# Performance work log

Measured on AMD Instinct MI355X. Metric: run time of the kernel, lower is better.

The kernel has to match this reference:

```python
import jax, jax.numpy as jnp
import numpy as np

# norse default LIFParameters
DT = 1e-3
TAU_SYN_INV = 200.0
TAU_MEM_INV = 100.0
V_LEAK = 0.0
V_TH = 1.0
V_RESET = 0.0


def heaviside(x):
    return (x > 0).astype(x.dtype)


def setup_inputs() -> dict:
    key = jax.random.key(0)
    ks = jax.random.split(key, 5)
    T, B, I, H, O = 14, 4096, 2048, 1024, 128
    x = (jax.random.uniform(ks[0], (T, B, I), dtype=jnp.float32) < 0.2).astype(jnp.float32)  # spike train
    w_in = jax.random.normal(ks[1], (H, I), dtype=jnp.float32) * (1.0 / np.sqrt(I))
    w_rec = jax.random.normal(ks[2], (H, H), dtype=jnp.float32) * (1.0 / np.sqrt(H))
    out_w = jax.random.normal(ks[3], (O, H), dtype=jnp.float32) * (1.0 / np.sqrt(H))
    out_b = jax.random.normal(ks[4], (O,), dtype=jnp.float32) * 0.01
    return {"x": x, "w_in": w_in, "w_rec": w_rec, "out_w": out_w, "out_b": out_b}


def reference(x, w_in, w_rec, out_w, out_b):
    T, B, _ = x.shape
    H = w_in.shape[0]
    z0 = jnp.zeros((B, H), dtype=x.dtype)
    v0 = jnp.full((B, H), V_LEAK, dtype=x.dtype)
    i0 = jnp.zeros((B, H), dtype=x.dtype)

    def step(carry, x_t):
        z, v, i = carry
        v_dec = v + DT * TAU_MEM_INV * ((V_LEAK - v) + i)   # membrane integration
        i_dec = i - DT * TAU_SYN_INV * i                    # synaptic decay
        z_new = heaviside(v_dec - V_TH)                     # spike
        v_new = (1.0 - z_new) * v_dec + z_new * V_RESET     # reset
        i_new = i_dec + x_t @ w_in.T + z @ w_rec.T          # input + recurrent current
        return (z_new, v_new, i_new), None

    (z_T, _, _), _ = jax.lax.scan(step, (z0, v0, i0), x)
    return z_T @ out_w.T + out_b
```

## Files before the change

kernel.cpp:

```cpp
#include <hip/hip_runtime.h>
#include <stdint.h>

#define T_STEPS 14
#define B_DIM   4096
#define I_DIM   2048
#define H_DIM   1024
#define O_DIM   128
#define K_TOT   3072

#define WSCALE_F 33554432.0f

typedef __bf16  bf16x8  __attribute__((ext_vector_type(8)));
typedef float   floatx4 __attribute__((ext_vector_type(4)));
typedef int     int4v   __attribute__((ext_vector_type(4)));
typedef int     int16v  __attribute__((ext_vector_type(16)));

__device__ __forceinline__ uint16_t f2bf_rne(float f) {
    uint32_t u = __float_as_uint(f);
    u += 0x7fffu + ((u >> 16) & 1u);
    return (uint16_t)(u >> 16);
}
__device__ __forceinline__ float bf2f(uint16_t h) {
    return __uint_as_float(((uint32_t)h) << 16);
}

__device__ __forceinline__ void gload_lds16(const void* g, void* l) {
    __builtin_amdgcn_global_load_lds((__attribute__((address_space(1))) void*)g,
                                     (__attribute__((address_space(3))) void*)l, 16, 0, 0);
}


__global__ void split_w_kernel(const float* __restrict__ w_in, const float* __restrict__ w_rec,
                               int8_t* __restrict__ WB) {
    int idx = blockIdx.x * 256 + threadIdx.x;
    int h = idx / K_TOT;
    int k = idx - h * K_TOT;
    float w = (k < I_DIM) ? w_in[(size_t)h * I_DIM + k]
                          : w_rec[(size_t)h * H_DIM + (k - I_DIM)];
    int W  = __float2int_rn(w * WSCALE_F);
    int d0 = (int8_t)(W & 0xFF);
    int r1 = (W - d0) >> 8;
    int d1 = (int8_t)(r1 & 0xFF);
    int d2 = (r1 - d1) >> 8;
    int nt = h >> 5, n32 = h & 31;
    int ktw = k >> 7, k128 = k & 127;
    int kk = k128 >> 5, half = (k128 >> 4) & 1, j = k128 & 15;
    int lane = half * 32 + n32;
    size_t base = (size_t)(nt * 24 + ktw) * 12288 + kk * 1024 + lane * 16 + j;
    WB[base] = (int8_t)d0; WB[base + 4096] = (int8_t)d1; WB[base + 8192] = (int8_t)d2;
}

__global__ void split_ow_kernel(const float* __restrict__ out_w, uint16_t* __restrict__ OW3) {
    int idx = blockIdx.x * 256 + threadIdx.x;
    float w = out_w[idx];
    uint16_t hi = f2bf_rne(w);
    float r1 = w - bf2f(hi);
    uint16_t mid = f2bf_rne(r1);
    float r2 = r1 - bf2f(mid);
    uint16_t lo = f2bf_rne(r2);
    const size_t S = (size_t)O_DIM * H_DIM;
    OW3[idx] = hi; OW3[idx + S] = mid; OW3[idx + 2 * S] = lo;
}

__global__ void cvt_x_kernel(const float* __restrict__ x, int8_t* __restrict__ xb) {
    size_t gid = (size_t)blockIdx.x * 256 + threadIdx.x;
    int g = (int)(gid & 1023);
    size_t chunk = gid >> 10;
    int kt   = (int)(chunk & 15);
    int mIdx = (int)((chunk >> 4) & 31);
    int t    = (int)(chunk >> 9);
    int group = g >> 8, kk = (g >> 6) & 3, lane = g & 63;
    int half = lane >> 5, row32 = lane & 31;
    int b = mIdx * 128 + group * 32 + row32;
    int k = kt * 128 + kk * 32 + half * 16;
    const float4* src = (const float4*)(x + ((size_t)t * B_DIM + b) * I_DIM + k);
    union { int8_t bytes[16]; int4v v; } u;
#pragma unroll
    for (int q = 0; q < 4; ++q) {
        float4 f = src[q];
        u.bytes[q * 4 + 0] = (int8_t)(f.x > 0.5f);
        u.bytes[q * 4 + 1] = (int8_t)(f.y > 0.5f);
        u.bytes[q * 4 + 2] = (int8_t)(f.z > 0.5f);
        u.bytes[q * 4 + 3] = (int8_t)(f.w > 0.5f);
    }
    ((int4v*)xb)[gid] = u.v;
}

__launch_bounds__(256, 4)
__global__ void lif_step_kernel(const int8_t* __restrict__ Xt,
                                const int8_t* __restrict__ Zin,
                                const int8_t* __restrict__ WB,
                                float2* __restrict__ VI,
                                int8_t* __restrict__ Zout,
                                uint16_t* __restrict__ Zbf, int t) {
    __shared__ int8_t sA[16384];
    __shared__ int8_t sB[12288];

    const int tid  = threadIdx.x;
    const int wave = tid >> 6, lane = tid & 63;
    const int lane32 = lane & 31, hl = lane >> 5;

    const int nt = blockIdx.x & 31, mIdx = blockIdx.x >> 5;
    const int mBase = mIdx * 128, nBase = nt * 32;

    int16v acc[3] = {};

    const int nIters = (t > 0) ? 24 : 16;

    for (int kt = 0; kt < nIters; ++kt) {
        __syncthreads();
        const int8_t* chunkA = (kt < 16)
            ? Xt  + ((size_t)mIdx * 16 + kt) * 16384
            : Zin + ((size_t)mIdx * 8 + (kt - 16)) * 16384;
#pragma unroll
        for (int j = 0; j < 4; ++j) {
            const int seg = j * 4 + wave;
            gload_lds16(chunkA + seg * 1024 + lane * 16, &sA[seg * 1024]);
        }
        const int8_t* chunkB = WB + (size_t)(nt * 24 + kt) * 12288;
#pragma unroll
        for (int j = 0; j < 3; ++j) {
            const int seg = j * 4 + wave;
            gload_lds16(chunkB + seg * 1024 + lane * 16, &sB[seg * 1024]);
        }
        __syncthreads();
#pragma unroll
        for (int kk = 0; kk < 4; ++kk) {
            int4v aF = *(const int4v*)&sA[wave * 4096 + kk * 1024 + lane * 16];
#pragma unroll
            for (int s = 0; s < 3; ++s) {
                int4v bF = *(const int4v*)&sB[s * 4096 + kk * 1024 + lane * 16];
                acc[s] = __builtin_amdgcn_mfma_i32_32x32x32_i8(aF, bF, acc[s], 0, 0, 0);
            }
        }
    }

    int8_t* zchunk = Zout + ((size_t)mIdx * 8 + (nt >> 2)) * 16384;
#pragma unroll
    for (int r = 0; r < 16; ++r) {
#pragma clang fp contract(off)
        float cur = (float)acc[2][r] * (1.0f / 512.0f)
                  + (float)acc[1][r] * (1.0f / 131072.0f)
                  + (float)acc[0][r] * (1.0f / 33554432.0f);
        int row = (r & 3) + 8 * (r >> 2) + 4 * hl;
        int b = mBase + wave * 32 + row;
        int h = nBase + lane32;
        size_t idx = (size_t)b * H_DIM + h;
        float v, ii;
        if (t == 0) { v = 0.0f; ii = 0.0f; }
        else        { float2 vi = VI[idx]; v = vi.x; ii = vi.y; }
        float v_dec = v + 0.1f * ((0.0f - v) + ii);
        float i_dec = ii - 0.2f * ii;
        bool z = (v_dec > 1.0f);
        float2 vi_new;
        vi_new.x = z ? 0.0f : v_dec;
        vi_new.y = i_dec + cur;
        VI[idx] = vi_new;
        if (t == T_STEPS - 1) {
            Zbf[idx] = z ? (uint16_t)0x3F80 : (uint16_t)0;
        } else {
            zchunk[wave * 4096 + (nt & 3) * 1024
                   + ((lane32 >> 4) * 32 + row) * 16 + (lane32 & 15)]
                = z ? (int8_t)1 : (int8_t)0;
        }
    }
}

__launch_bounds__(256)
__global__ void out_gemm_kernel(const uint16_t* __restrict__ Zfin,
                                const uint16_t* __restrict__ OW3,
                                const float* __restrict__ out_b,
                                float* __restrict__ out) {
    __shared__ uint16_t sA[16 * 32];
    __shared__ uint16_t sB[3][128 * 32];

    const int tid  = threadIdx.x;
    const int wave = tid >> 6, lane = tid & 63;
    const int quad = lane >> 4, col = lane & 15;

    const int mBase = blockIdx.x * 16;

    floatx4 acc[2] = {};

    const int ldRow = lane >> 2;
    const int ldCol = (lane & 3) * 8;

    for (int kt = 0; kt < H_DIM / 32; ++kt) {
        const int kb = kt * 32;
        __syncthreads();
        if (wave == 0) {
            const uint16_t* g = Zfin + (size_t)(mBase + ldRow) * H_DIM + kb + ldCol;
            gload_lds16(g, &sA[0]);
        }
#pragma unroll
        for (int s = 0; s < 3; ++s) {
            const uint16_t* wsrc = OW3 + (size_t)s * O_DIM * H_DIM;
#pragma unroll
            for (int j = 0; j < 2; ++j) {
                const int rseg = j * 4 + wave;
                const uint16_t* g = wsrc + (size_t)(rseg * 16 + ldRow) * H_DIM + kb + ldCol;
                gload_lds16(g, &sB[s][rseg * 16 * 32]);
            }
        }
        __syncthreads();

        bf16x8 aF = *reinterpret_cast<const bf16x8*>(&sA[col * 32 + quad * 8]);
#pragma unroll
        for (int s = 0; s < 3; ++s) {
#pragma unroll
            for (int ni = 0; ni < 2; ++ni) {
                int row = wave * 32 + ni * 16 + col;
                bf16x8 bF = *reinterpret_cast<const bf16x8*>(&sB[s][row * 32 + quad * 8]);
                acc[ni] = __builtin_amdgcn_mfma_f32_16x16x32_bf16(aF, bF, acc[ni], 0, 0, 0);
            }
        }
    }

    {
#pragma clang fp contract(off)
#pragma unroll
        for (int ni = 0; ni < 2; ++ni)
#pragma unroll
            for (int r = 0; r < 4; ++r) {
                int b = mBase + quad * 4 + r;
                int h = wave * 32 + ni * 16 + col;
                out[(size_t)b * O_DIM + h] = acc[ni][r] + out_b[h];
            }
    }
}

extern "C" void kernel_launch(void* const* d_in, const int* in_sizes, int n_in,
                              void* d_out, int out_size, void* d_ws, size_t ws_size,
                              hipStream_t stream) {
    const float* x     = (const float*)d_in[0];
    const float* w_in  = (const float*)d_in[1];
    const float* w_rec = (const float*)d_in[2];
    const float* out_w = (const float*)d_in[3];
    const float* out_b = (const float*)d_in[4];
    float* out = (float*)d_out;

    char* ws = (char*)d_ws;
    size_t off = 0;
    int8_t*   WB   = (int8_t*)(ws + off);   off += (size_t)3 * H_DIM * K_TOT;
    uint16_t* OW3  = (uint16_t*)(ws + off); off += (size_t)3 * O_DIM * H_DIM * 2;
    int8_t*   Xall = (int8_t*)(ws + off);   off += (size_t)T_STEPS * B_DIM * I_DIM;
    uint16_t* Zbf  = (uint16_t*)(ws + off); off += (size_t)B_DIM * H_DIM * 2;
    int8_t*   Z0   = (int8_t*)(ws + off);   off += (size_t)B_DIM * H_DIM;
    int8_t*   Z1   = (int8_t*)(ws + off);   off += (size_t)B_DIM * H_DIM;
    float2*   VI   = (float2*)(ws + off);   off += (size_t)B_DIM * H_DIM * 8;

    split_w_kernel<<<(H_DIM * K_TOT) / 256, 256, 0, stream>>>(w_in, w_rec, WB);
    split_ow_kernel<<<(O_DIM * H_DIM) / 256, 256, 0, stream>>>(out_w, OW3);
    cvt_x_kernel<<<(int)(((size_t)T_STEPS * B_DIM * I_DIM / 16) / 256), 256, 0, stream>>>(x, Xall);

    int8_t* zbuf[2] = { Z0, Z1 };
    for (int t = 0; t < T_STEPS; ++t) {
        lif_step_kernel<<<dim3(1024), 256, 0, stream>>>(
            Xall + (size_t)t * 32 * 16 * 16384, zbuf[t & 1], WB, VI,
            zbuf[(t + 1) & 1], Zbf, t);
    }
    out_gemm_kernel<<<B_DIM / 16, 256, 0, stream>>>(Zbf, OW3, out_b, out);
}
```

Before: 1.375 ms.

## Fuse LIF timesteps into one persistent cooperative kernel with grid sync

```diff
diff --git a/kernel.cpp b/kernel.cpp
--- a/kernel.cpp
+++ b/kernel.cpp
@@ -1,5 +1,8 @@
 #include <hip/hip_runtime.h>
+#include <hip/hip_cooperative_groups.h>
 #include <stdint.h>
+
+namespace cg = cooperative_groups;
 
 #define T_STEPS 14
 #define B_DIM   4096
@@ -84,6 +87,116 @@
         u.bytes[q * 4 + 3] = (int8_t)(f.w > 0.5f);
     }
     ((int4v*)xb)[gid] = u.v;
+}
+
+__launch_bounds__(256, 4)
+__global__ void lif_persist_kernel(const int8_t* __restrict__ Xall,
+                                   const int8_t* __restrict__ WB,
+                                   int8_t* __restrict__ Z0,
+                                   int8_t* __restrict__ Z1,
+                                   uint16_t* __restrict__ Zbf) {
+    __shared__ int8_t sA[16384];
+    __shared__ int8_t sB[12288];
+
+    const int tid  = threadIdx.x;
+    const int wave = tid >> 6, lane = tid & 63;
+    const int lane32 = lane & 31, hl = lane >> 5;
+
+    const int nt = blockIdx.x & 31, mIdx = blockIdx.x >> 5;
+    const int mBase = mIdx * 128, nBase = nt * 32;
+
+    float vmem[16], isyn[16];
+#pragma unroll
+    for (int r = 0; r < 16; ++r) { vmem[r] = 0.0f; isyn[r] = 0.0f; }
+
+    int8_t* zA = Z0;
+    int8_t* zB = Z1;
+
+    for (int t = 0; t < T_STEPS; ++t) {
+        int16v acc[3] = {};
+        const int8_t* Xt = Xall + (size_t)t * ((size_t)B_DIM * I_DIM);
+
+        for (int kt = 0; kt < 16; ++kt) {
+            __syncthreads();
+            const int8_t* chunkA = Xt + ((size_t)mIdx * 16 + kt) * 16384;
+#pragma unroll
+            for (int j = 0; j < 4; ++j) {
+                const int seg = j * 4 + wave;
+                gload_lds16(chunkA + seg * 1024 + lane * 16, &sA[seg * 1024]);
+            }
+            const int8_t* chunkB = WB + (size_t)(nt * 24 + kt) * 12288;
+#pragma unroll
+            for (int j = 0; j < 3; ++j) {
+                const int seg = j * 4 + wave;
+                gload_lds16(chunkB + seg * 1024 + lane * 16, &sB[seg * 1024]);
+            }
+            __syncthreads();
+#pragma unroll
+            for (int kk = 0; kk < 4; ++kk) {
+                int4v aF = *(const int4v*)&sA[wave * 4096 + kk * 1024 + lane * 16];
+#pragma unroll
+                for (int s = 0; s < 3; ++s) {
+                    int4v bF = *(const int4v*)&sB[s * 4096 + kk * 1024 + lane * 16];
+                    acc[s] = __builtin_amdgcn_mfma_i32_32x32x32_i8(aF, bF, acc[s], 0, 0, 0);
+                }
+            }
+        }
+
+        if (t > 0) {
+            cg::this_grid().sync();
+            for (int kt = 0; kt < 8; ++kt) {
+                __syncthreads();
+                const int8_t* chunkA = zA + ((size_t)mIdx * 8 + kt) * 16384;
+#pragma unroll
+                for (int j = 0; j < 4; ++j) {
+                    const int seg = j * 4 + wave;
+                    gload_lds16(chunkA + seg * 1024 + lane * 16, &sA[seg * 1024]);
+                }
+                const int8_t* chunkB = WB + (size_t)(nt * 24 + 16 + kt) * 12288;
+#pragma unroll
+                for (int j = 0; j < 3; ++j) {
+                    const int seg = j * 4 + wave;
+                    gload_lds16(chunkB + seg * 1024 + lane * 16, &sB[seg * 1024]);
+                }
+                __syncthreads();
+#pragma unroll
+                for (int kk = 0; kk < 4; ++kk) {
+                    int4v aF = *(const int4v*)&sA[wave * 4096 + kk * 1024 + lane * 16];
+#pragma unroll
+                    for (int s = 0; s < 3; ++s) {
+                        int4v bF = *(const int4v*)&sB[s * 4096 + kk * 1024 + lane * 16];
+                        acc[s] = __builtin_amdgcn_mfma_i32_32x32x32_i8(aF, bF, acc[s], 0, 0, 0);
+                    }
+                }
+            }
+        }
+
+        int8_t* zchunk = zB + ((size_t)mIdx * 8 + (nt >> 2)) * 16384;
+#pragma unroll
+        for (int r = 0; r < 16; ++r) {
+#pragma clang fp contract(off)
+            float cur = (float)acc[2][r] * (1.0f / 512.0f)
+                      + (float)acc[1][r] * (1.0f / 131072.0f)
+                      + (float)acc[0][r] * (1.0f / 33554432.0f);
+            int row = (r & 3) + 8 * (r >> 2) + 4 * hl;
+            float v_dec = vmem[r] + 0.1f * ((0.0f - vmem[r]) + isyn[r]);
+            float i_dec = isyn[r] - 0.2f * isyn[r];
+            bool z = (v_dec > 1.0f);
+            vmem[r] = z ? 0.0f : v_dec;
+            isyn[r] = i_dec + cur;
+            if (t == T_STEPS - 1) {
+                int b = mBase + wave * 32 + row;
+                int h = nBase + lane32;
+                Zbf[(size_t)b * H_DIM + h] = z ? (uint16_t)0x3F80 : (uint16_t)0;
+            } else {
+                zchunk[wave * 4096 + (nt & 3) * 1024
+                       + ((lane32 >> 4) * 32 + row) * 16 + (lane32 & 15)]
+                    = z ? (int8_t)1 : (int8_t)0;
+            }
+        }
+
+        int8_t* tmp = zA; zA = zB; zB = tmp;
+    }
 }
 
 __launch_bounds__(256, 4)
@@ -253,11 +366,30 @@
     split_ow_kernel<<<(O_DIM * H_DIM) / 256, 256, 0, stream>>>(out_w, OW3);
     cvt_x_kernel<<<(int)(((size_t)T_STEPS * B_DIM * I_DIM / 16) / 256), 256, 0, stream>>>(x, Xall);
 
-    int8_t* zbuf[2] = { Z0, Z1 };
-    for (int t = 0; t < T_STEPS; ++t) {
-        lif_step_kernel<<<dim3(1024), 256, 0, stream>>>(
-            Xall + (size_t)t * 32 * 16 * 16384, zbuf[t & 1], WB, VI,
-            zbuf[(t + 1) & 1], Zbf, t);
-    }
+    static int coop_ok = -1;
+    if (coop_ok < 0) {
+        int dev = 0, v = 0;
+        (void)hipGetDevice(&dev);
+        if (hipDeviceGetAttribute(&v, hipDeviceAttributeCooperativeLaunch, dev) != hipSuccess) v = 0;
+        coop_ok = v;
+    }
+
+    bool launched = false;
+    if (coop_ok) {
+        void* args[] = { (void*)&Xall, (void*)&WB, (void*)&Z0, (void*)&Z1, (void*)&Zbf };
+        hipError_t e = hipLaunchCooperativeKernel((const void*)lif_persist_kernel,
+                                                  dim3(1024), dim3(256), args, 0, stream);
+        if (e == hipSuccess) launched = true;
+        else coop_ok = 0;
+    }
+    if (!launched) {
+        int8_t* zbuf[2] = { Z0, Z1 };
+        for (int t = 0; t < T_STEPS; ++t) {
+            lif_step_kernel<<<dim3(1024), 256, 0, stream>>>(
+                Xall + (size_t)t * B_DIM * I_DIM, zbuf[t & 1], WB, VI,
+                zbuf[(t + 1) & 1], Zbf, t);
+        }
+    }
+
     out_gemm_kernel<<<B_DIM / 16, 256, 0, stream>>>(Zbf, OW3, out_b, out);
 }
```

Measured after the change: 1.349 ms. No clear change (-1.9%).
